# Optimization experiments

Measured on AMD Instinct MI355X. Metric: run time of the kernel, lower is better.

## Reference

```python
import jax, jax.numpy as jnp
import numpy as np

N_NODES = 20000
N_EDGES = 80000
D = 128       # in_dim_node == in_dim_edge == hidden dims
ITERS = 15    # mp_iterations
EPS = 1e-5    # torch LayerNorm default eps


def _mlp(h, W0, b0, W1, b1, W2, b2, gamma, beta):
    """Linear-ReLU-Linear-ReLU-Linear-LayerNorm (hidden_layers=2)."""
    h = jax.nn.relu(h @ W0 + b0)
    h = jax.nn.relu(h @ W1 + b1)
    h = h @ W2 + b2
    mu = jnp.mean(h, axis=-1, keepdims=True)
    var = jnp.var(h, axis=-1, keepdims=True)
    return gamma * (h - mu) * jax.lax.rsqrt(var + EPS) + beta


def setup_inputs() -> dict:
    key = jax.random.key(0)
    ks = iter(jax.random.split(key, 32))

    def lin(fi, fo):
        bnd = 1.0 / np.sqrt(fi)
        W = jax.random.uniform(next(ks), (ITERS, fi, fo), minval=-bnd, maxval=bnd, dtype=jnp.float32)
        b = jax.random.uniform(next(ks), (ITERS, fo), minval=-bnd, maxval=bnd, dtype=jnp.float32)
        return W, b

    x = jax.random.normal(next(ks), (N_NODES, D), dtype=jnp.float32)
    edge_attr = jax.random.normal(next(ks), (N_EDGES, D), dtype=jnp.float32)
    edge_index = jax.random.randint(next(ks), (2, N_EDGES), 0, N_NODES)

    eW0, eB0 = lin(3 * D, D)   # edge MLP input = cat(src, dest, edge) = 384
    eW1, eB1 = lin(D, D)
    eW2, eB2 = lin(D, D)
    nW0, nB0 = lin(2 * D, D)   # node MLP input = cat(x, agg) = 256
    nW1, nB1 = lin(D, D)
    nW2, nB2 = lin(D, D)
    ones = jnp.ones((ITERS, D), jnp.float32)
    zeros = jnp.zeros((ITERS, D), jnp.float32)

    return dict(x=x, edge_attr=edge_attr,
                eW0=eW0, eB0=eB0, eW1=eW1, eB1=eB1, eW2=eW2, eB2=eB2, eG=ones, eBeta=zeros,
                nW0=nW0, nB0=nB0, nW1=nW1, nB1=nB1, nW2=nW2, nB2=nB2, nG=ones, nBeta=zeros,
                edge_index=edge_index)


def reference(x, edge_attr, eW0, eB0, eW1, eB1, eW2, eB2, eG, eBeta,
              nW0, nB0, nW1, nB1, nW2, nB2, nG, nBeta, edge_index):
    row, col = edge_index[0], edge_index[1]
    n = x.shape[0]
    params = (eW0, eB0, eW1, eB1, eW2, eB2, eG, eBeta,
              nW0, nB0, nW1, nB1, nW2, nB2, nG, nBeta)

    def step(carry, p):
        xc, ec = carry
        (ew0, eb0, ew1, eb1, ew2, eb2, eg, ebt,
         nw0, nb0, nw1, nb1, nw2, nb2, ng, nbt) = p
        # EdgeProcessor: gather + MLP, then FullResidualConnection (add previous)
        e_in = jnp.concatenate([xc[row], xc[col], ec], axis=-1)        # [E, 3D]
        ec = _mlp(e_in, ew0, eb0, ew1, eb1, ew2, eb2, eg, ebt) + ec
        # NodeProcessor: scatter_sum over destination nodes + MLP + residual
        agg = jax.ops.segment_sum(ec, col, num_segments=n)             # [N, D]
        n_in = jnp.concatenate([xc, agg], axis=-1)                     # [N, 2D]
        xc = _mlp(n_in, nw0, nb0, nw1, nb1, nw2, nb2, ng, nbt) + xc
        return (xc, ec), None

    (x, edge_attr), _ = jax.lax.scan(step, (x, edge_attr), params)
    return x, edge_attr
```

## Files before the change

kernel.cpp:

```cpp
#include <hip/hip_runtime.h>
#include <hip/hip_bf16.h>

typedef __hip_bfloat16 bf16;
typedef __attribute__((ext_vector_type(8))) short short8;
typedef __attribute__((ext_vector_type(4))) float f32x4;

#define NN 20000
#define NE 80000
#define DD 128
#define NITER 15
#define HSTRIDE 136

__device__ inline void gload16(const void* g, void* l) {
  __builtin_amdgcn_global_load_lds(
      (const __attribute__((address_space(1))) void*)g,
      (__attribute__((address_space(3))) void*)l, 16, 0, 0);
}

__device__ inline void waitVm(int n) {
  switch (n) {
    case 0: asm volatile("s_waitcnt vmcnt(0)" ::: "memory"); break;
    case 1: asm volatile("s_waitcnt vmcnt(1)" ::: "memory"); break;
    case 2: asm volatile("s_waitcnt vmcnt(2)" ::: "memory"); break;
    case 3: asm volatile("s_waitcnt vmcnt(3)" ::: "memory"); break;
    case 4: asm volatile("s_waitcnt vmcnt(4)" ::: "memory"); break;
    case 5: asm volatile("s_waitcnt vmcnt(5)" ::: "memory"); break;
    default: asm volatile("s_waitcnt vmcnt(6)" ::: "memory"); break;
  }
}

__device__ inline float bfbits2f(unsigned int hi16) {
  union { unsigned int u; float f; } c; c.u = hi16; return c.f;
}

__device__ inline float readin(const void* p, size_t i, int fl) {
  return fl ? (float)((const bf16*)p)[i] : ((const float*)p)[i];
}

__global__ void detzero_kernel(const unsigned short* __restrict__ x,
                               int* __restrict__ counts, int* __restrict__ flag) {
  const int bid = blockIdx.x, t = threadIdx.x;
  if (bid < 79) {
    int i = bid * 256 + t;
    if (i < NN) counts[i] = 0;
    return;
  }
  __shared__ int cs[256], ct[256];
  int sane = 0, tot = 0;
  for (int i = 2 * t; i < 16384; i += 512) {
    unsigned short v = x[i];
    int e = (v >> 7) & 0xFF;
    tot++;
    if (v == 0 || (e >= 80 && e <= 170)) sane++;
  }
  cs[t] = sane; ct[t] = tot;
  __syncthreads();
  for (int o = 128; o > 0; o >>= 1) {
    if (t < o) { cs[t] += cs[t + o]; ct[t] += ct[t + o]; }
    __syncthreads();
  }
  if (t == 0) *flag = (cs[0] * 10 > ct[0] * 7) ? 1 : 0;
}

#define CX  (NN * DD)
#define CE  (NE * DD)
#define CW0 (NITER * 384 * DD)
#define CW1 (NITER * 128 * DD)
#define CNW0 (NITER * 256 * DD)
#define CB  (NITER * DD)
#define BX0 CX
#define BX1 (BX0 + CE)
#define BX2 (BX1 + 10 * CB)

struct CvtP {
  const void *x, *e;
  bf16 *xb, *eb;
  const void* bs[10];
  float* bd[10];
  const int* flag;
};

__global__ void convert_all(CvtP P) {
  const int fl = *P.flag;
  const int gstride = gridDim.x * 256;
  for (int i = blockIdx.x * 256 + threadIdx.x; i < BX2; i += gstride) {
    if (i < BX0) {
      P.xb[i] = (bf16)readin(P.x, i, fl);
    } else if (i < BX1) {
      P.eb[i - BX0] = (bf16)readin(P.e, i - BX0, fl);
    } else {
      int j = i - BX1;
      int b = j / CB, r = j - b * CB;
      P.bd[b][r] = readin(P.bs[b], r, fl);
    }
  }
}

struct WtP {
  const void* w[6];
  bf16* wt[6];
  const int* flag;
};

__global__ void wtrans_kernel(WtP P) {
  __shared__ float tile[32][33];
  const int fl = *P.flag;
  const int bid = blockIdx.x;
  int w, rem;
  if      (bid < 720)  { w = 0; rem = bid; }
  else if (bid < 960)  { w = 1; rem = bid - 720; }
  else if (bid < 1200) { w = 2; rem = bid - 960; }
  else if (bid < 1680) { w = 3; rem = bid - 1200; }
  else if (bid < 1920) { w = 4; rem = bid - 1680; }
  else                 { w = 5; rem = bid - 1920; }
  const int K = (w == 0) ? 384 : (w == 3) ? 256 : 128;
  const int nkt    = K >> 5;
  const int per_it = nkt << 2;
  const int it = rem / per_it;
  const int r2 = rem - it * per_it;
  const int k0 = (r2 >> 2) << 5;
  const int n0 = (r2 & 3) << 5;

  const int tx = threadIdx.x & 31, ty = threadIdx.x >> 5;
  const size_t base = (size_t)it * K * DD;

#pragma unroll
  for (int p = 0; p < 4; p++) {
    const int k = k0 + ty + 8 * p;
    tile[ty + 8 * p][tx] = readin(P.w[w], base + (size_t)k * DD + n0 + tx, fl);
  }
  __syncthreads();
#pragma unroll
  for (int p = 0; p < 4; p++) {
    const int n = n0 + ty + 8 * p;
    const int k = k0 + tx;
    const int q = (k >> 3) & 3;
    const int kp = (k & ~24) | (((q ^ ((n >> 1) & 3)) & 3) << 3);
    P.wt[w][base + (size_t)n * K + kp] = (bf16)tile[tx][ty + 8 * p];
  }
}

template<int K0, int AMODE, int NW, int MI>
__global__ __launch_bounds__(NW * 64, MI == 2 ? 3 : 4) void fused_mlp(
    const bf16* S0b,
    const bf16* S1b,
    const int*  __restrict__ eidx,
    const bf16* __restrict__ W0t, const bf16* __restrict__ W1t,
    const bf16* __restrict__ W2t,
    const float* __restrict__ b0, const float* __restrict__ b1,
    const float* __restrict__ b2,
    const float* __restrict__ gamma, const float* __restrict__ beta,
    bf16* st, int M)
{
  constexpr int NS1  = K0 / 32;
  constexpr int RPW  = 16 * MI;
  constexpr int ROWS = NW * RPW;
  constexpr int DN   = 2;
  __shared__ __align__(16) bf16 Bls[2][128 * 32];
  __shared__ __align__(16) bf16 Hls[ROWS * HSTRIDE];

  const int tid  = threadIdx.x;
  const int lane = tid & 63;
  const int wv   = tid >> 6;
  const int l15  = lane & 15, quad = lane >> 4;
  const int m0   = blockIdx.x * ROWS;
  const int scol = tid >> 2;
  const int sk8  = (tid & 3) * 8;

  int rowm[MI], ir[MI], ic[MI];
#pragma unroll
  for (int g = 0; g < MI; g++) {
    rowm[g] = min(m0 + wv * RPW + g * 16 + l15, M - 1);
    ir[g] = 0; ic[g] = 0;
    if (AMODE == 1) { ir[g] = eidx[rowm[g]]; ic[g] = eidx[NE + rowm[g]]; }
  }

  auto dmaW = [&](const bf16* W, int K, int kk, int buf) {
    gload16(W + (size_t)scol * K + kk + sk8,        &Bls[buf][scol * 32 + sk8]);
    gload16(W + (size_t)(scol + 64) * K + kk + sk8, &Bls[buf][(scol + 64) * 32 + sk8]);
  };
  auto gatherA = [&](int g, int kk, short8* a) {
    const int ks = (kk & 127) + quad * 8;
    const bf16* base;
    if (AMODE == 1) {
      const int seg = kk >> 7;
      base = (seg == 0) ? S0b + (size_t)ir[g] * DD
           : (seg == 1) ? S0b + (size_t)ic[g] * DD
                        : S1b + (size_t)rowm[g] * DD;
    } else {
      base = (kk >> 7) ? S1b + (size_t)rowm[g] * DD
                       : S0b + (size_t)rowm[g] * DD;
    }
    *a = *(const short8*)(base + ks);
  };

  auto readB = [&](int buf, short8* bfr) {
#pragma unroll
    for (int ni = 0; ni < 8; ni++) {
      const int r = ni * 16 + l15;
      bfr[ni] = *(const short8*)&Bls[buf][r * 32 + ((quad ^ ((r >> 1) & 3)) & 3) * 8];
    }
  };

  f32x4 acc[MI][8];
  auto zacc = [&]() {
#pragma unroll
    for (int g = 0; g < MI; g++)
#pragma unroll
      for (int j = 0; j < 8; j++) acc[g][j] = (f32x4){0.f, 0.f, 0.f, 0.f};
  };
  auto slabMfmaA = [&](short8* a, int buf) {
    short8 bfr[8];
    readB(buf, bfr);
#pragma unroll
    for (int g = 0; g < MI; g++)
#pragma unroll
      for (int ni = 0; ni < 8; ni++)
        acc[g][ni] = __builtin_amdgcn_mfma_f32_16x16x32_bf16(a[g], bfr[ni], acc[g][ni], 0, 0, 0);
  };
  auto slabMfmaH = [&](int kk, int buf) {
    short8 bfr[8];
    readB(buf, bfr);
#pragma unroll
    for (int g = 0; g < MI; g++) {
      short8 a = *(const short8*)&Hls[(wv * RPW + g * 16 + l15) * HSTRIDE + kk + quad * 8];
#pragma unroll
      for (int ni = 0; ni < 8; ni++)
        acc[g][ni] = __builtin_amdgcn_mfma_f32_16x16x32_bf16(a, bfr[ni], acc[g][ni], 0, 0, 0);
    }
  };
  auto writeH = [&](const float* bias) {
    float bv[8];
#pragma unroll
    for (int ni = 0; ni < 8; ni++) bv[ni] = bias[ni * 16 + l15];
#pragma unroll
    for (int g = 0; g < MI; g++)
#pragma unroll
      for (int r = 0; r < 4; r++) {
        const int row = wv * RPW + g * 16 + quad * 4 + r;
#pragma unroll
        for (int ni = 0; ni < 8; ni++)
          Hls[row * HSTRIDE + ni * 16 + l15] = (bf16)fmaxf(acc[g][ni][r] + bv[ni], 0.f);
      }
  };

  zacc();
  short8 aCur[MI], aNxt[MI];
  dmaW(W0t, K0, 0, 0);
#pragma unroll
  for (int g = 0; g < MI; g++) gatherA(g, 0, &aCur[g]);
#pragma unroll
  for (int s = 0; s < NS1; s++) {
    int cnt;
    if (s + 1 < NS1) {
      dmaW(W0t, K0, (s + 1) * 32, (s + 1) & 1);
#pragma unroll
      for (int g = 0; g < MI; g++) gatherA(g, (s + 1) * 32, &aNxt[g]);
      cnt = MI + DN + MI;
    } else {
      dmaW(W1t, 128, 0, NS1 & 1);
      cnt = MI + DN;
    }
    waitVm(cnt);
    __builtin_amdgcn_s_barrier();
    __builtin_amdgcn_sched_barrier(0);
    slabMfmaA(aCur, s & 1);
    __builtin_amdgcn_sched_barrier(0);
    __builtin_amdgcn_s_barrier();
#pragma unroll
    for (int g = 0; g < MI; g++) aCur[g] = aNxt[g];
  }
  writeH(b0);

  zacc();
#pragma unroll
  for (int s = 0; s < 4; s++) {
    if (s < 3) dmaW(W1t, 128, (s + 1) * 32, (NS1 + s + 1) & 1);
    else       dmaW(W2t, 128, 0,            (NS1 + 4) & 1);
    waitVm(DN);
    __builtin_amdgcn_s_barrier();
    __builtin_amdgcn_sched_barrier(0);
    slabMfmaH(s * 32, (NS1 + s) & 1);
    __builtin_amdgcn_sched_barrier(0);
    __builtin_amdgcn_s_barrier();
  }
  writeH(b1);

  zacc();
#pragma unroll
  for (int s = 0; s < 4; s++) {
    int cnt = 0;
    if (s < 3) { dmaW(W2t, 128, (s + 1) * 32, (NS1 + 4 + s + 1) & 1); cnt = DN; }
    waitVm(cnt);
    __builtin_amdgcn_s_barrier();
    __builtin_amdgcn_sched_barrier(0);
    slabMfmaH(s * 32, (NS1 + 4 + s) & 1);
    if (s < 3) {
      __builtin_amdgcn_sched_barrier(0);
      __builtin_amdgcn_s_barrier();
    }
  }

  float bv[8], gv[8], btv[8];
#pragma unroll
  for (int ni = 0; ni < 8; ni++) {
    const int col = ni * 16 + l15;
    bv[ni] = b2[col]; gv[ni] = gamma[col]; btv[ni] = beta[col];
  }
#pragma unroll
  for (int g = 0; g < MI; g++) {
#pragma unroll
    for (int r = 0; r < 4; r++) {
      float a = 0.f, bq = 0.f;
#pragma unroll
      for (int ni = 0; ni < 8; ni++) {
        const float v = acc[g][ni][r] + bv[ni];
        a += v; bq += v * v;
      }
#pragma unroll
      for (int off = 1; off < 16; off <<= 1) {
        a  += __shfl_xor(a, off);
        bq += __shfl_xor(bq, off);
      }
      const float mu = a * (1.0f / 128.0f);
      const float var = fmaxf(bq * (1.0f / 128.0f) - mu * mu, 0.0f);
      const float rs = rsqrtf(var + 1e-5f);
      const int m = m0 + wv * RPW + g * 16 + quad * 4 + r;
      if (m < M) {
#pragma unroll
        for (int ni = 0; ni < 8; ni++) {
          const int col = ni * 16 + l15;
          const float v = acc[g][ni][r] + bv[ni];
          const float lnv = (v - mu) * rs * gv[ni] + btv[ni];
          const size_t idx = (size_t)m * DD + col;
          st[idx] = (bf16)(lnv + (float)st[idx]);
        }
      }
    }
  }
}

__global__ void hist_kernel(const int* __restrict__ eidx, int* __restrict__ counts) {
  int e = blockIdx.x * 256 + threadIdx.x;
  if (e < NE) atomicAdd(&counts[eidx[NE + e]], 1);
}

__global__ void scan_kernel(const int* __restrict__ counts, int* __restrict__ offs,
                            int* __restrict__ cursor) {
  __shared__ int sums[1024];
  const int t = threadIdx.x;
  const int base = t * 20;
  int local[20];
  int s = 0;
  for (int i = 0; i < 20; i++) {
    int idx = base + i;
    int c = (idx < NN) ? counts[idx] : 0;
    local[i] = s; s += c;
  }
  sums[t] = s;
  __syncthreads();
  for (int off = 1; off < 1024; off <<= 1) {
    int v = 0;
    if (t >= off) v = sums[t - off];
    __syncthreads();
    if (t >= off) sums[t] += v;
    __syncthreads();
  }
  int excl = (t == 0) ? 0 : sums[t - 1];
  for (int i = 0; i < 20; i++) {
    int idx = base + i;
    if (idx < NN) { offs[idx] = excl + local[i]; cursor[idx] = 0; }
  }
  if (t == 1023) offs[NN] = sums[1023];
}

__global__ void fill_kernel(const int* __restrict__ eidx, const int* __restrict__ offs,
                            int* __restrict__ cursor, int* __restrict__ sorted) {
  int e = blockIdx.x * 256 + threadIdx.x;
  if (e < NE) {
    int n = eidx[NE + e];
    int p = atomicAdd(&cursor[n], 1);
    sorted[offs[n] + p] = e;
  }
}

__global__ void aggregate_kernel(const bf16* __restrict__ eb, const int* __restrict__ offs,
                                 const int* __restrict__ sorted, bf16* __restrict__ aggb) {
  const int node = blockIdx.x * 4 + (threadIdx.x >> 6);
  const int lane = threadIdx.x & 63;
  if (node >= NN) return;
  const int s = offs[node], t = offs[node + 1];
  float a0 = 0.f, a1 = 0.f;
  for (int i = s; i < t; i++) {
    const int e = sorted[i];
    unsigned int v = *(const unsigned int*)(eb + (size_t)e * DD + 2 * lane);
    a0 += bfbits2f(v << 16);
    a1 += bfbits2f(v & 0xFFFF0000u);
  }
  bf16 o0 = (bf16)a0, o1 = (bf16)a1;
  unsigned int pack = (unsigned int)(*(unsigned short*)&o0)
                    | ((unsigned int)(*(unsigned short*)&o1) << 16);
  *(unsigned int*)(aggb + (size_t)node * DD + 2 * lane) = pack;
}

__global__ void outwb_kernel(const bf16* __restrict__ xb, const bf16* __restrict__ eb,
                             void* __restrict__ out, const int* __restrict__ flag) {
  int i = blockIdx.x * 256 + threadIdx.x;
  const int nx = NN * DD, total = (NN + NE) * DD;
  if (i < total) {
    bf16 v = (i < nx) ? xb[i] : eb[i - nx];
    if (*flag) ((bf16*)out)[i] = v;
    else       ((float*)out)[i] = (float)v;
  }
}

extern "C" void kernel_launch(void* const* d_in, const int* in_sizes, int n_in,
                              void* d_out, int out_size, void* d_ws, size_t ws_size,
                              hipStream_t stream) {
  const int* eidx = (const int*)d_in[18];

  char* ws = (char*)d_ws;
  size_t off = 0;
  auto alloc = [&](size_t bytes) -> char* {
    char* p = ws + off;
    off = (off + bytes + 255) & ~(size_t)255;
    return p;
  };

  bf16* xb   = (bf16*)alloc((size_t)NN * DD * 2);
  bf16* eb   = (bf16*)alloc((size_t)NE * DD * 2);
  bf16* aggb = (bf16*)alloc((size_t)NN * DD * 2);
  bf16* eW0t = (bf16*)alloc((size_t)CW0 * 2);
  bf16* eW1t = (bf16*)alloc((size_t)CW1 * 2);
  bf16* eW2t = (bf16*)alloc((size_t)CW1 * 2);
  bf16* nW0t = (bf16*)alloc((size_t)CNW0 * 2);
  bf16* nW1t = (bf16*)alloc((size_t)CW1 * 2);
  bf16* nW2t = (bf16*)alloc((size_t)CW1 * 2);
  float* bf_[10];
  for (int i = 0; i < 10; i++) bf_[i] = (float*)alloc(CB * 4);
  int* counts = (int*)alloc((size_t)NN * 4);
  int* cursor = (int*)alloc((size_t)NN * 4);
  int* offs   = (int*)alloc((size_t)(NN + 1) * 4);
  int* sorted = (int*)alloc((size_t)NE * 4);
  int* flag   = (int*)alloc(4);

  detzero_kernel<<<80, 256, 0, stream>>>((const unsigned short*)d_in[0], counts, flag);

  CvtP C;
  C.x = d_in[0]; C.e = d_in[1];
  C.xb = xb; C.eb = eb;
  const int bsrc_idx[10] = {3, 5, 7, 8, 9, 11, 13, 15, 16, 17};
  for (int i = 0; i < 10; i++) { C.bs[i] = d_in[bsrc_idx[i]]; C.bd[i] = bf_[i]; }
  C.flag = flag;
  convert_all<<<2048, 256, 0, stream>>>(C);

  WtP W;
  W.w[0] = d_in[2];  W.w[1] = d_in[4];  W.w[2] = d_in[6];
  W.w[3] = d_in[10]; W.w[4] = d_in[12]; W.w[5] = d_in[14];
  W.wt[0] = eW0t; W.wt[1] = eW1t; W.wt[2] = eW2t;
  W.wt[3] = nW0t; W.wt[4] = nW1t; W.wt[5] = nW2t;
  W.flag = flag;
  wtrans_kernel<<<2160, 256, 0, stream>>>(W);

  hist_kernel<<<(NE + 255) / 256, 256, 0, stream>>>(eidx, counts);
  scan_kernel<<<1, 1024, 0, stream>>>(counts, offs, cursor);
  fill_kernel<<<(NE + 255) / 256, 256, 0, stream>>>(eidx, offs, cursor, sorted);

  const int egrid = NE / 128;
  const int ngrid = (NN + 63) / 64;

  for (int t = 0; t < NITER; t++) {
    fused_mlp<384, 1, 4, 2><<<egrid, 256, 0, stream>>>(
        xb, eb, eidx,
        eW0t + (size_t)t * 384 * DD, eW1t + (size_t)t * 128 * DD,
        eW2t + (size_t)t * 128 * DD,
        bf_[0] + t * DD, bf_[1] + t * DD, bf_[2] + t * DD,
        bf_[3] + t * DD, bf_[4] + t * DD, eb, NE);
    aggregate_kernel<<<(NN + 3) / 4, 256, 0, stream>>>(eb, offs, sorted, aggb);
    fused_mlp<256, 2, 4, 1><<<ngrid, 256, 0, stream>>>(
        xb, aggb, nullptr,
        nW0t + (size_t)t * 256 * DD, nW1t + (size_t)t * 128 * DD,
        nW2t + (size_t)t * 128 * DD,
        bf_[5] + t * DD, bf_[6] + t * DD, bf_[7] + t * DD,
        bf_[8] + t * DD, bf_[9] + t * DD, xb, NN);
  }

  outwb_kernel<<<((NN + NE) * DD + 255) / 256, 256, 0, stream>>>(xb, eb, d_out, flag);
}
```

Before: 1.065 ms.

## Merge setup kernels, deepen A-gather prefetch, fuse output writeback into last iteration

Merges the input conversion and weight transpose kernels into one launch, with block ranges selecting the work. Deepens the A-operand gather in the first GEMM stage to prefetch two slabs ahead, at the cost of extra registers. Drops the separate output writeback kernel: in the last iteration the fused MLP epilogue stores results straight to the output buffer in bf16 or fp32. These remove two launches and an extra pass over node and edge data, but add a branch and a flag load to the epilogue.

```diff
diff --git a/kernel.cpp b/kernel.cpp
--- a/kernel.cpp
+++ b/kernel.cpp
@@ -71,48 +71,46 @@
 #define BX0 CX
 #define BX1 (BX0 + CE)
 #define BX2 (BX1 + 10 * CB)
+#define CVT_BLOCKS 2048
+#define WT_TILES   2160
 
 struct CvtP {
   const void *x, *e;
   bf16 *xb, *eb;
   const void* bs[10];
   float* bd[10];
-  const int* flag;
-};
-
-__global__ void convert_all(CvtP P) {
-  const int fl = *P.flag;
-  const int gstride = gridDim.x * 256;
-  for (int i = blockIdx.x * 256 + threadIdx.x; i < BX2; i += gstride) {
-    if (i < BX0) {
-      P.xb[i] = (bf16)readin(P.x, i, fl);
-    } else if (i < BX1) {
-      P.eb[i - BX0] = (bf16)readin(P.e, i - BX0, fl);
-    } else {
-      int j = i - BX1;
-      int b = j / CB, r = j - b * CB;
-      P.bd[b][r] = readin(P.bs[b], r, fl);
-    }
-  }
-}
-
-struct WtP {
   const void* w[6];
   bf16* wt[6];
   const int* flag;
 };
 
-__global__ void wtrans_kernel(WtP P) {
-  __shared__ float tile[32][33];
+__global__ void convert_all(CvtP P) {
   const int fl = *P.flag;
   const int bid = blockIdx.x;
+  if (bid < CVT_BLOCKS) {
+    const int gstride = CVT_BLOCKS * 256;
+    for (int i = bid * 256 + threadIdx.x; i < BX2; i += gstride) {
+      if (i < BX0) {
+        P.xb[i] = (bf16)readin(P.x, i, fl);
+      } else if (i < BX1) {
+        P.eb[i - BX0] = (bf16)readin(P.e, i - BX0, fl);
+      } else {
+        int j = i - BX1;
+        int b = j / CB, r = j - b * CB;
+        P.bd[b][r] = readin(P.bs[b], r, fl);
+      }
+    }
+    return;
+  }
+  __shared__ float tile[32][33];
+  const int tb = bid - CVT_BLOCKS;
   int w, rem;
-  if      (bid < 720)  { w = 0; rem = bid; }
-  else if (bid < 960)  { w = 1; rem = bid - 720; }
-  else if (bid < 1200) { w = 2; rem = bid - 960; }
-  else if (bid < 1680) { w = 3; rem = bid - 1200; }
-  else if (bid < 1920) { w = 4; rem = bid - 1680; }
-  else                 { w = 5; rem = bid - 1920; }
+  if      (tb < 720)  { w = 0; rem = tb; }
+  else if (tb < 960)  { w = 1; rem = tb - 720; }
+  else if (tb < 1200) { w = 2; rem = tb - 960; }
+  else if (tb < 1680) { w = 3; rem = tb - 1200; }
+  else if (tb < 1920) { w = 4; rem = tb - 1680; }
+  else                { w = 5; rem = tb - 1920; }
   const int K = (w == 0) ? 384 : (w == 3) ? 256 : 128;
   const int nkt    = K >> 5;
   const int per_it = nkt << 2;
@@ -150,7 +148,7 @@
     const float* __restrict__ b0, const float* __restrict__ b1,
     const float* __restrict__ b2,
     const float* __restrict__ gamma, const float* __restrict__ beta,
-    bf16* st, int M)
+    bf16* st, int M, void* dout, const int* dflag)
 {
   constexpr int NS1  = K0 / 32;
   constexpr int RPW  = 16 * MI;
@@ -245,22 +243,22 @@
   };
 
   zacc();
-  short8 aCur[MI], aNxt[MI];
+  short8 aCur[MI], aNxt[MI], aNx2[MI];
   dmaW(W0t, K0, 0, 0);
 #pragma unroll
   for (int g = 0; g < MI; g++) gatherA(g, 0, &aCur[g]);
 #pragma unroll
+  for (int g = 0; g < MI; g++) gatherA(g, 32, &aNxt[g]);
+#pragma unroll
   for (int s = 0; s < NS1; s++) {
-    int cnt;
-    if (s + 1 < NS1) {
-      dmaW(W0t, K0, (s + 1) * 32, (s + 1) & 1);
-#pragma unroll
-      for (int g = 0; g < MI; g++) gatherA(g, (s + 1) * 32, &aNxt[g]);
-      cnt = MI + DN + MI;
-    } else {
-      dmaW(W1t, 128, 0, NS1 & 1);
-      cnt = MI + DN;
-    }
+    if (s + 1 < NS1) dmaW(W0t, K0, (s + 1) * 32, (s + 1) & 1);
+    else             dmaW(W1t, 128, 0,            NS1 & 1);
+    if (s + 2 < NS1) {
+#pragma unroll
+      for (int g = 0; g < MI; g++) gatherA(g, (s + 2) * 32, &aNx2[g]);
+    }
+    const int cnt = (s <= NS1 - 3) ? (2 * MI + DN)
+                  : (s == NS1 - 2) ? (MI + DN) : DN;
     waitVm(cnt);
     __builtin_amdgcn_s_barrier();
     __builtin_amdgcn_sched_barrier(0);
@@ -268,7 +266,7 @@
     __builtin_amdgcn_sched_barrier(0);
     __builtin_amdgcn_s_barrier();
 #pragma unroll
-    for (int g = 0; g < MI; g++) aCur[g] = aNxt[g];
+    for (int g = 0; g < MI; g++) { aCur[g] = aNxt[g]; aNxt[g] = aNx2[g]; }
   }
   writeH(b0);
 
@@ -301,6 +299,7 @@
     }
   }
 
+  const int ofl = dout ? *dflag : 0;
   float bv[8], gv[8], btv[8];
 #pragma unroll
   for (int ni = 0; ni < 8; ni++) {
@@ -333,7 +332,13 @@
           const float v = acc[g][ni][r] + bv[ni];
           const float lnv = (v - mu) * rs * gv[ni] + btv[ni];
           const size_t idx = (size_t)m * DD + col;
-          st[idx] = (bf16)(lnv + (float)st[idx]);
+          bf16 stv = (bf16)(lnv + (float)st[idx]);
+          st[idx] = stv;
+          if (dout) {
+            const size_t oidx = (AMODE == 1 ? (size_t)NN * DD : 0) + idx;
+            if (ofl) ((bf16*)dout)[oidx] = stv;
+            else     ((float*)dout)[oidx] = (float)stv;
+          }
         }
       }
     }
@@ -401,17 +406,6 @@
   unsigned int pack = (unsigned int)(*(unsigned short*)&o0)
                     | ((unsigned int)(*(unsigned short*)&o1) << 16);
   *(unsigned int*)(aggb + (size_t)node * DD + 2 * lane) = pack;
-}
-
-__global__ void outwb_kernel(const bf16* __restrict__ xb, const bf16* __restrict__ eb,
-                             void* __restrict__ out, const int* __restrict__ flag) {
-  int i = blockIdx.x * 256 + threadIdx.x;
-  const int nx = NN * DD, total = (NN + NE) * DD;
-  if (i < total) {
-    bf16 v = (i < nx) ? xb[i] : eb[i - nx];
-    if (*flag) ((bf16*)out)[i] = v;
-    else       ((float*)out)[i] = (float)v;
-  }
 }
 
 extern "C" void kernel_launch(void* const* d_in, const int* in_sizes, int n_in,
@@ -451,16 +445,12 @@
   C.xb = xb; C.eb = eb;
   const int bsrc_idx[10] = {3, 5, 7, 8, 9, 11, 13, 15, 16, 17};
   for (int i = 0; i < 10; i++) { C.bs[i] = d_in[bsrc_idx[i]]; C.bd[i] = bf_[i]; }
+  C.w[0] = d_in[2];  C.w[1] = d_in[4];  C.w[2] = d_in[6];
+  C.w[3] = d_in[10]; C.w[4] = d_in[12]; C.w[5] = d_in[14];
+  C.wt[0] = eW0t; C.wt[1] = eW1t; C.wt[2] = eW2t;
+  C.wt[3] = nW0t; C.wt[4] = nW1t; C.wt[5] = nW2t;
   C.flag = flag;
-  convert_all<<<2048, 256, 0, stream>>>(C);
-
-  WtP W;
-  W.w[0] = d_in[2];  W.w[1] = d_in[4];  W.w[2] = d_in[6];
-  W.w[3] = d_in[10]; W.w[4] = d_in[12]; W.w[5] = d_in[14];
-  W.wt[0] = eW0t; W.wt[1] = eW1t; W.wt[2] = eW2t;
-  W.wt[3] = nW0t; W.wt[4] = nW1t; W.wt[5] = nW2t;
-  W.flag = flag;
-  wtrans_kernel<<<2160, 256, 0, stream>>>(W);
+  convert_all<<<CVT_BLOCKS + WT_TILES, 256, 0, stream>>>(C);
 
   hist_kernel<<<(NE + 255) / 256, 256, 0, stream>>>(eidx, counts);
   scan_kernel<<<1, 1024, 0, stream>>>(counts, offs, cursor);
@@ -470,20 +460,19 @@
   const int ngrid = (NN + 63) / 64;
 
   for (int t = 0; t < NITER; t++) {
+    void* eout = (t == NITER - 1) ? d_out : nullptr;
     fused_mlp<384, 1, 4, 2><<<egrid, 256, 0, stream>>>(
         xb, eb, eidx,
         eW0t + (size_t)t * 384 * DD, eW1t + (size_t)t * 128 * DD,
         eW2t + (size_t)t * 128 * DD,
         bf_[0] + t * DD, bf_[1] + t * DD, bf_[2] + t * DD,
-        bf_[3] + t * DD, bf_[4] + t * DD, eb, NE);
+        bf_[3] + t * DD, bf_[4] + t * DD, eb, NE, eout, flag);
     aggregate_kernel<<<(NN + 3) / 4, 256, 0, stream>>>(eb, offs, sorted, aggb);
     fused_mlp<256, 2, 4, 1><<<ngrid, 256, 0, stream>>>(
         xb, aggb, nullptr,
         nW0t + (size_t)t * 256 * DD, nW1t + (size_t)t * 128 * DD,
         nW2t + (size_t)t * 128 * DD,
         bf_[5] + t * DD, bf_[6] + t * DD, bf_[7] + t * DD,
-        bf_[8] + t * DD, bf_[9] + t * DD, xb, NN);
-  }
-
-  outwb_kernel<<<((NN + NE) * DD + 255) / 256, 256, 0, stream>>>(xb, eb, d_out, flag);
-}
+        bf_[8] + t * DD, bf_[9] + t * DD, xb, NN, eout, flag);
+  }
+}
```

After: 1.196 ms. 12.3% more time.
